# Performance work log

Measured on AMD Instinct MI355X. Metric: run time of the kernel, lower is better.

## Reference

```python
import jax, jax.numpy as jnp
import numpy as np

# LeNet-5 custom connectivity between S2 (6 ch) and C3 (16 ch): MAP[i, o] = 1 if input ch i feeds output ch o
MAP_INFO = np.array([
    [1, 0, 0, 0, 1, 1, 1, 0, 0, 1, 1, 1, 1, 0, 1, 1],
    [1, 1, 0, 0, 0, 1, 1, 1, 0, 0, 1, 1, 1, 1, 0, 1],
    [1, 1, 1, 0, 0, 0, 1, 1, 1, 0, 0, 1, 0, 1, 1, 1],
    [0, 1, 1, 1, 0, 0, 1, 1, 1, 1, 0, 0, 1, 0, 1, 1],
    [0, 0, 1, 1, 1, 0, 0, 1, 1, 1, 1, 0, 1, 1, 0, 1],
    [0, 0, 0, 1, 1, 1, 0, 0, 1, 1, 1, 1, 0, 1, 1, 1],
], dtype=np.float32)  # [6, 16]

SCALE = 1.7159
SLOPE = 2.0 / 3.0


def _conv(x, w):
    # x: [B, Cin, H, W], w: [Cout, Cin, kh, kw], VALID padding, stride 1
    return jax.lax.conv_general_dilated(
        x, w, window_strides=(1, 1), padding='VALID',
        dimension_numbers=('NCHW', 'OIHW', 'NCHW'))


def _subsample(x, w, b):
    # 2x2 average pool then per-channel affine (trainable scale/bias)
    B, C, H, W = x.shape
    p = x.reshape(B, C, H // 2, 2, W // 2, 2).mean(axis=(3, 5))
    return p * w[None, :, None, None] + b[None, :, None, None]


def _act(x):
    return SCALE * jnp.tanh(SLOPE * x)


def setup_inputs() -> dict:
    key = jax.random.key(0)
    ks = jax.random.split(key, 16)
    B = 8192

    def unif(k, shape, fan_in):
        return (jax.random.uniform(k, shape, dtype=jnp.float32) * 4.8 - 2.4) / fan_in

    x = jax.random.normal(ks[0], (B, 1, 32, 32), dtype=jnp.float32)
    c1_w = unif(ks[1], (6, 1, 5, 5), 25 * 1)
    c1_b = jax.random.uniform(ks[2], (6,), dtype=jnp.float32) * 0.1
    s2_w = unif(ks[3], (6,), 4)
    s2_b = jax.random.uniform(ks[4], (6,), dtype=jnp.float32)
    c3_w = unif(ks[5], (16, 6, 5, 5), 25 * 6)
    c3_b = jax.random.uniform(ks[6], (16,), dtype=jnp.float32) * 0.1
    s4_w = unif(ks[7], (16,), 4)
    s4_b = jax.random.uniform(ks[8], (16,), dtype=jnp.float32)
    c5_w = unif(ks[9], (120, 16, 5, 5), 25 * 16)
    c5_b = jax.random.uniform(ks[10], (120,), dtype=jnp.float32) * 0.1
    f6_w = unif(ks[11], (84, 120), 120)
    f6_b = jax.random.uniform(ks[12], (84,), dtype=jnp.float32) * 0.1
    rbf_w = jax.random.uniform(ks[13], (84, 10), dtype=jnp.float32)
    return dict(x=x, c1_w=c1_w, c1_b=c1_b, s2_w=s2_w, s2_b=s2_b,
                c3_w=c3_w, c3_b=c3_b, s4_w=s4_w, s4_b=s4_b,
                c5_w=c5_w, c5_b=c5_b, f6_w=f6_w, f6_b=f6_b, rbf_w=rbf_w)


def reference(x, c1_w, c1_b, s2_w, s2_b, c3_w, c3_b, s4_w, s4_b,
              c5_w, c5_b, f6_w, f6_b, rbf_w):
    # C1: 1->6 conv5, replicate padding 2 -> [B,6,32,32]
    xp = jnp.pad(x, ((0, 0), (0, 0), (2, 2), (2, 2)), mode='edge')
    h = _conv(xp, c1_w) + c1_b[None, :, None, None]
    # S2 + squashing act -> [B,6,16,16]
    h = _act(_subsample(h, s2_w, s2_b))
    # C3: sparse-connectivity conv expressed as dense conv with masked weights -> [B,16,12,12]
    mask = jnp.asarray(MAP_INFO.T)[:, :, None, None]  # [16,6,1,1]
    h = _conv(h, c3_w * mask) + c3_b[None, :, None, None]
    # S4 + act -> [B,16,6,6]
    h = _act(_subsample(h, s4_w, s4_b))
    # C5: 16->120 conv5 -> [B,120,1,1]
    h = _conv(h, c5_w) + c5_b[None, :, None, None]
    h = h.reshape(-1, 120)
    # F6 + act -> [B,84]
    h = _act(h @ f6_w.T + f6_b)
    # RBF output: squared euclidean distance to class prototypes -> [B,10]
    out = jnp.sum((h[:, :, None] - rbf_w[None, :, :]) ** 2, axis=1)
    return out
```

## Files before the change

### kernel.cpp

```cpp
#include <hip/hip_runtime.h>
#include <math.h>

typedef _Float16 h16;
typedef h16  h8v __attribute__((ext_vector_type(8)));
typedef h16  h4v __attribute__((ext_vector_type(4)));
typedef h16  h2v __attribute__((ext_vector_type(2)));
typedef float f4v __attribute__((ext_vector_type(4)));
typedef unsigned int u32;

#define WS_B1   0
#define WS_B3   8
#define WS_KB1  24
#define WS_W3H  408
#define WS_W5H  2712
#define WS_F6H  29336
#define WS_RBFH 35480
#define WS_PSQ  36248

#define L_B3    0
#define L_C5B   64
#define L_F6B   544
#define L_S2H   880
#define L_A5    880
#define L_HBH   880
#define L_XPAD  14704
#define L_S4    14704
#define L_A6    14704
#define L_GUARD 19888
#define LDS_TOTAL 20080

__device__ const unsigned char MASK16[16] = {7,14,28,56,49,35,15,30,60,57,51,39,27,54,45,63};

__device__ __forceinline__ float squash(float x) {
    float E = __expf(1.33333333f * x);
    return 1.7159f - 3.4318f * __builtin_amdgcn_rcpf(1.0f + E);
}

__device__ __forceinline__ void slot_to_uv(int c, int& u, int& v) {
    u = -1; v = 0;
    if (c < 32) {
        int q = c >> 3, j = c & 7;
        if (j < 6)       { u = q;     v = j; }
        else if (q == 2) { u = 4;     v = j - 6; }
        else if (q == 3) { u = 5;     v = j - 6; }
    } else {
        int cc = c - 32, q = cc >> 2, j = cc & 3;
        if (q == 0)      { u = 4;     v = 2 + j; }
        else if (q == 1) { u = 5;     v = 2 + j; }
    }
}

__global__ __launch_bounds__(256) void prep_kernel(
    const float* __restrict__ c1_w, const float* __restrict__ c1_b,
    const float* __restrict__ s2_w, const float* __restrict__ s2_b,
    const float* __restrict__ c3_w, const float* __restrict__ c3_b,
    const float* __restrict__ s4_w, const float* __restrict__ s4_b,
    const float* __restrict__ c5_w, const float* __restrict__ f6_w,
    const float* __restrict__ rbf_w,
    float* __restrict__ ws)
{
    const int gid = blockIdx.x * 256 + threadIdx.x;
    const int gstr = gridDim.x * 256;
    if (gid < 6)  ws[WS_B1 + gid] = s2_w[gid] * c1_b[gid] + s2_b[gid];
    if (gid < 16) ws[WS_B3 + gid] = s4_w[gid] * c3_b[gid] + s4_b[gid];
    h16* KB1 = (h16*)(ws + WS_KB1);
    for (int idx = gid; idx < 768; idx += gstr) {
        int n = idx / 48, c = idx - n * 48;
        int u, v; slot_to_uv(c, u, v);
        float val = 0.f;
        if (n < 6 && u >= 0) {
            float s = 0.f;
            #pragma unroll
            for (int dy = 0; dy < 2; ++dy)
                #pragma unroll
                for (int dx = 0; dx < 2; ++dx) {
                    int ky = u - dy, kx = v - dx;
                    if (ky >= 0 && ky < 5 && kx >= 0 && kx < 5)
                        s += c1_w[(n * 5 + ky) * 5 + kx];
                }
            val = 0.25f * s * s2_w[n];
        }
        KB1[idx] = (h16)val;
    }
    h16* W3H = (h16*)(ws + WS_W3H);
    for (int idx = gid; idx < 4608; idx += gstr) {
        int i = idx / 768, r = idx - i * 768;
        int n = r / 48, c = r - n * 48;
        int u, v; slot_to_uv(c, u, v);
        float val = 0.f;
        if (u >= 0) {
            float s = 0.f;
            #pragma unroll
            for (int dy = 0; dy < 2; ++dy)
                #pragma unroll
                for (int dx = 0; dx < 2; ++dx) {
                    int ky = u - dy, kx = v - dx;
                    if (ky >= 0 && ky < 5 && kx >= 0 && kx < 5)
                        s += c3_w[((n * 6 + i) * 5 + ky) * 5 + kx];
                }
            val = ((MASK16[n] >> i) & 1) ? 0.25f * s4_w[n] * s : 0.f;
        }
        W3H[idx] = (h16)val;
    }
    h16* W5H = (h16*)(ws + WS_W5H);
    for (int idx = gid; idx < 53248; idx += gstr) {
        int kb = idx >> 12, rr = idx & 4095;
        int n = rr >> 5, k = rr & 31;
        int kg = kb * 32 + k;
        int i = kg / 26, r = kg - i * 26;
        float val = (n < 120 && r < 25) ? c5_w[n * 400 + i * 25 + r] : 0.f;
        W5H[idx] = (h16)val;
    }
    h16* F6H = (h16*)(ws + WS_F6H);
    for (int idx = gid; idx < 12288; idx += gstr) {
        int n = idx >> 7, k = idx & 127;
        float val = (n < 84 && k < 120) ? f6_w[n * 120 + k] : 0.f;
        F6H[idx] = (h16)val;
    }
    h16* RBFH = (h16*)(ws + WS_RBFH);
    for (int idx = gid; idx < 1536; idx += gstr) {
        int n = idx / 96, k = idx - n * 96;
        float val = (n < 10 && k < 84) ? -2.f * rbf_w[k * 10 + n] : 0.f;
        RBFH[idx] = (h16)val;
    }
    if (gid < 10) {
        float s = 0.f;
        for (int k = 0; k < 84; ++k) {
            float pv = (float)(h16)rbf_w[k * 10 + gid];
            s += pv * pv;
        }
        ws[WS_PSQ + gid] = s;
    }
}

__global__ __launch_bounds__(256, 8) void lenet_kernel(
    const float* __restrict__ x,
    const float* __restrict__ c5_b, const float* __restrict__ f6_b,
    const float* __restrict__ ws,
    float* __restrict__ out)
{
    __shared__ __align__(16) char smem[LDS_TOTAL];
    float* s_b3  = (float*)(smem + L_B3);
    float* s_c5b = (float*)(smem + L_C5B);
    float* s_f6b = (float*)(smem + L_F6B);
    h16*  XPAD   = (h16*)(smem + L_XPAD);
    h16*  S2H    = (h16*)(smem + L_S2H);
    h16*  S4     = (h16*)(smem + L_S4);
    h16*  A5     = (h16*)(smem + L_A5);
    h16*  A6     = (h16*)(smem + L_A6);
    h16*  HBH    = (h16*)(smem + L_HBH);

    const int tid  = threadIdx.x;
    const int wave = __builtin_amdgcn_readfirstlane(tid >> 6);
    const int lane = tid & 63;
    const int quad = lane >> 4;
    const int lr   = lane & 15;

    if (tid < 16)  s_b3[tid] = ws[WS_B3 + tid];
    if (tid < 120) s_c5b[tid] = c5_b[tid];
    if (tid < 84)  s_f6b[tid] = f6_b[tid];
    if (tid < 48)  ((u32*)(smem + L_GUARD))[tid] = 0u;
    const float* xb = x + (size_t)blockIdx.x * 4096;
    const h16* KB1 = (const h16*)(ws + WS_KB1);
    h8v w1a = *(const h8v*)(KB1 + lr * 48 + quad * 8);
    h4v w1b = *(const h4v*)(KB1 + lr * 48 + 32 + quad * 4);
    float b1v = ws[WS_B1 + (lr < 6 ? lr : 0)];
    float psqv = ws[WS_PSQ + (lr < 10 ? lr : 0)];

    auto stageA = [&](int s) {
        #pragma unroll
        for (int k = 0; k < 2; ++k) {
            int idx = tid + k * 256;
            int im = idx >> 8;
            int r  = (idx >> 3) & 31;
            int c4 = idx & 7;
            float4 v = *(const float4*)(xb + (2 * s + im) * 1024 + r * 32 + c4 * 4);
            h2v p0; p0.x = (h16)v.x; p0.y = (h16)v.y;
            h2v p1; p1.x = (h16)v.z; p1.y = (h16)v.w;
            h16* d = XPAD + im * 1296 + (r + 2) * 36 + (4 * c4 + 2);
            *(h2v*)(d)     = p0;
            *(h2v*)(d + 2) = p1;
        }
        #pragma unroll
        for (int k = 0; k < 3; ++k) {
            int e = tid + k * 256;
            if (e < 544) {
                int im = (e >= 272) ? 1 : 0;
                int h = e - 272 * im;
                int u, v;
                if (h < 144) { int q = h / 36; u = (q < 2) ? q : 32 + q; v = h - q * 36; }
                else { int g = h - 144; u = 2 + (g >> 2); int q = g & 3; v = (q < 2) ? q : 32 + q; }
                int sr = min(max(u - 2, 0), 31), sc = min(max(v - 2, 0), 31);
                XPAD[im * 1296 + u * 36 + v] = (h16)xb[(2 * s + im) * 1024 + sr * 32 + sc];
            }
        }
    };

    auto stageB = [&](int s) {
        const h16* bp = XPAD + (wave >> 1) * 1296 + (wave & 1) * 576 + 2 * lr;
        h16* s2base = S2H + (s * 2 + (wave >> 1)) * 1728 + lr * 288 + (wave & 1) * 144 + quad * 4;
        #pragma unroll
        for (int tt = 0; tt < 8; ++tt) {
            const u32* bq = (const u32*)bp + quad * 18;
            union { u32 u[4]; h8v h; } av;
            av.u[0] = bq[0];  av.u[1] = bq[1];
            av.u[2] = bq[2];  av.u[3] = bq[36];
            f4v acc = {b1v, b1v, b1v, b1v};
            acc = __builtin_amdgcn_mfma_f32_16x16x32_f16(av.h, w1a, acc, 0, 0, 0);
            union { u32 u[2]; h4v h; } av2;
            av2.u[0] = bq[73]; av2.u[1] = bq[74];
            acc = __builtin_amdgcn_mfma_f32_16x16x16f16(av2.h, w1b, acc, 0, 0, 0);
            if (lr < 6) {
                h2v q0; q0.x = (h16)squash(acc[0]); q0.y = (h16)squash(acc[1]);
                h2v q1; q1.x = (h16)squash(acc[2]); q1.y = (h16)squash(acc[3]);
                *(h2v*)(s2base + tt * 18)     = q0;
                *(h2v*)(s2base + tt * 18 + 2) = q1;
            }
            bp += 72;
        }
    };

    stageA(0);
    __syncthreads();
    stageB(0);
    __syncthreads();
    stageA(1);
    __syncthreads();
    stageB(1);
    __syncthreads();

    f4v cacc0, cacc1, cacc2;
    const bool w0 = (wave == 0);
    {
        const h16* W3H = (const h16*)(ws + WS_W3H);
        int baseh0, baseh1, baseh2;
        {
            int m0 = wave * 16 + lr;
            int i0 = m0 / 36, p0 = m0 - i0 * 36;
            baseh0 = i0 * 1728 + (2 * (p0 / 6)) * 18 + 2 * (p0 % 6);
            int m1 = (wave + 4) * 16 + lr;
            int i1 = m1 / 36, p1 = m1 - i1 * 36;
            baseh1 = i1 * 1728 + (2 * (p1 / 6)) * 18 + 2 * (p1 % 6);
            int m2 = 128 + lr;
            int i2 = m2 / 36, p2 = m2 - i2 * 36;
            baseh2 = i2 * 1728 + (2 * (p2 / 6)) * 18 + 2 * (p2 % 6);
        }
        float b3v = s_b3[lr];
        f4v cinit = {b3v, b3v, b3v, b3v};
        cacc0 = cinit; cacc1 = cinit; cacc2 = cinit;
        #pragma unroll
        for (int i = 0; i < 6; ++i) {
            const h16* bbase = W3H + i * 768 + lr * 48;
            h8v w3a = *(const h8v*)(bbase + quad * 8);
            h4v w3b = *(const h4v*)(bbase + 32 + quad * 4);
            {
                const u32* cq = (const u32*)(S2H + baseh0 + i * 288) + quad * 9;
                union { u32 u[4]; h8v h; } av;
                av.u[0] = cq[0];  av.u[1] = cq[1];
                av.u[2] = cq[2];  av.u[3] = cq[18];
                cacc0 = __builtin_amdgcn_mfma_f32_16x16x32_f16(av.h, w3a, cacc0, 0, 0, 0);
                union { u32 u[2]; h4v h; } av2;
                av2.u[0] = cq[37]; av2.u[1] = cq[38];
                cacc0 = __builtin_amdgcn_mfma_f32_16x16x16f16(av2.h, w3b, cacc0, 0, 0, 0);
            }
            {
                const u32* cq = (const u32*)(S2H + baseh1 + i * 288) + quad * 9;
                union { u32 u[4]; h8v h; } av;
                av.u[0] = cq[0];  av.u[1] = cq[1];
                av.u[2] = cq[2];  av.u[3] = cq[18];
                cacc1 = __builtin_amdgcn_mfma_f32_16x16x32_f16(av.h, w3a, cacc1, 0, 0, 0);
                union { u32 u[2]; h4v h; } av2;
                av2.u[0] = cq[37]; av2.u[1] = cq[38];
                cacc1 = __builtin_amdgcn_mfma_f32_16x16x16f16(av2.h, w3b, cacc1, 0, 0, 0);
            }
            if (w0) {
                const u32* cq = (const u32*)(S2H + baseh2 + i * 288) + quad * 9;
                union { u32 u[4]; h8v h; } av;
                av.u[0] = cq[0];  av.u[1] = cq[1];
                av.u[2] = cq[2];  av.u[3] = cq[18];
                cacc2 = __builtin_amdgcn_mfma_f32_16x16x32_f16(av.h, w3a, cacc2, 0, 0, 0);
                union { u32 u[2]; h4v h; } av2;
                av2.u[0] = cq[37]; av2.u[1] = cq[38];
                cacc2 = __builtin_amdgcn_mfma_f32_16x16x16f16(av2.h, w3b, cacc2, 0, 0, 0);
            }
        }
    }

    const h16* W5H = (const h16*)(ws + WS_W5H);
    h8v bf0c = *(const h8v*)(W5H + (wave * 32 + lr) * 32 + quad * 8);
    h8v bf1c = *(const h8v*)(W5H + (wave * 32 + 16 + lr) * 32 + quad * 8);

    {
        #pragma unroll
        for (int r = 0; r < 4; ++r) {
            int m = wave * 16 + quad * 4 + r;
            int img = m / 36, pos = m - img * 36;
            S4[img * 672 + lr * 42 + pos] = (h16)squash(cacc0[r]);
        }
        #pragma unroll
        for (int r = 0; r < 4; ++r) {
            int m = (wave + 4) * 16 + quad * 4 + r;
            int img = m / 36, pos = m - img * 36;
            S4[img * 672 + lr * 42 + pos] = (h16)squash(cacc1[r]);
        }
        if (w0) {
            #pragma unroll
            for (int r = 0; r < 4; ++r) {
                int m = 128 + quad * 4 + r;
                int img = m / 36, pos = m - img * 36;
                S4[img * 672 + lr * 42 + pos] = (h16)squash(cacc2[r]);
            }
        }
    }
    __syncthreads();

    {
        int m = tid >> 4, i = tid & 15;
        int img = m >> 2, q = m & 3, qy = q >> 1, qx = q & 1;
        const h16* s4b = S4 + img * 672 + i * 42 + qy * 6 + qx;
        u32* dst = (u32*)(A5 + m * 424 + i * 26);
        #pragma unroll
        for (int w = 0; w < 12; ++w) {
            int k0 = 2 * w, k1 = 2 * w + 1;
            union { h2v h; u32 u; } p;
            p.h.x = s4b[(k0 / 5) * 6 + (k0 % 5)];
            p.h.y = s4b[(k1 / 5) * 6 + (k1 % 5)];
            dst[w] = p.u;
        }
        {
            union { h2v h; u32 u; } p;
            p.h.x = s4b[28];
            p.h.y = (h16)0.f;
            dst[12] = p.u;
        }
    }
    __syncthreads();

    {
        h8v af0c = *(const h8v*)(A5 + lr * 424 + quad * 8);
        float c5b0 = s_c5b[wave * 32 + lr];
        float c5b1 = s_c5b[wave * 32 + 16 + lr];
        f4v dacc0 = {c5b0, c5b0, c5b0, c5b0};
        f4v dacc1 = {c5b1, c5b1, c5b1, c5b1};
        #pragma unroll
        for (int i = 0; i < 13; ++i) {
            h8v bf0n, bf1n, af0n;
            if (i < 12) {
                bf0n = *(const h8v*)(W5H + (i + 1) * 4096 + (wave * 32 + lr) * 32 + quad * 8);
                bf1n = *(const h8v*)(W5H + (i + 1) * 4096 + (wave * 32 + 16 + lr) * 32 + quad * 8);
                af0n = *(const h8v*)(A5 + lr * 424 + (i + 1) * 32 + quad * 8);
            }
            dacc0 = __builtin_amdgcn_mfma_f32_16x16x32_f16(af0c, bf0c, dacc0, 0, 0, 0);
            dacc1 = __builtin_amdgcn_mfma_f32_16x16x32_f16(af0c, bf1c, dacc1, 0, 0, 0);
            if (i < 12) { bf0c = bf0n; bf1c = bf1n; af0c = af0n; }
        }
        if (tid < 64) {
            int m = tid >> 2, j = tid & 3;
            *(u32*)(A6 + m * 136 + 120 + 2 * j) = 0u;
        }
        {
            int n0 = wave * 32 + lr;
            if (n0 < 120) {
                int tt = n0 / 30, cb = (n0 - tt * 30) * 4;
                #pragma unroll
                for (int r = 0; r < 4; ++r) {
                    int m = quad * 4 + r;
                    A6[((m >> 2) * 4 + tt) * 136 + cb + (m & 3)] = (h16)dacc0[r];
                }
            }
            int n1 = wave * 32 + 16 + lr;
            if (n1 < 120) {
                int tt = n1 / 30, cb = (n1 - tt * 30) * 4;
                #pragma unroll
                for (int r = 0; r < 4; ++r) {
                    int m = quad * 4 + r;
                    A6[((m >> 2) * 4 + tt) * 136 + cb + (m & 3)] = (h16)dacc1[r];
                }
            }
        }
    }

    const h16* F6H = (const h16*)(ws + WS_F6H);
    const int wv2 = (wave < 2) ? wave + 4 : wave;
    h8v eb0c = *(const h8v*)(F6H + (wave * 16 + lr) * 128 + quad * 8);
    h8v eb1c = *(const h8v*)(F6H + (wv2 * 16 + lr) * 128 + quad * 8);
    __syncthreads();

    if (tid < 96) {
        int m = tid / 6, j = tid - m * 6;
        ((u32*)HBH)[m * 48 + 42 + j] = 0u;
    }

    {
        h8v a8c = *(const h8v*)(A6 + lr * 136 + quad * 8);
        float f60 = s_f6b[wave * 16 + lr];
        f4v eacc0 = {f60, f60, f60, f60};
        f4v eacc1 = {};
        const bool w2 = (wave < 2);
        if (w2) {
            int n1 = (wave + 4) * 16 + lr;
            float f61 = (n1 < 84) ? s_f6b[n1] : 0.f;
            eacc1[0] = f61; eacc1[1] = f61; eacc1[2] = f61; eacc1[3] = f61;
        }
        #pragma unroll
        for (int kc = 0; kc < 4; ++kc) {
            h8v eb0n, eb1n, a8n;
            if (kc < 3) {
                eb0n = *(const h8v*)(F6H + (wave * 16 + lr) * 128 + (kc + 1) * 32 + quad * 8);
                eb1n = *(const h8v*)(F6H + (wv2 * 16 + lr) * 128 + (kc + 1) * 32 + quad * 8);
                a8n  = *(const h8v*)(A6 + lr * 136 + (kc + 1) * 32 + quad * 8);
            }
            eacc0 = __builtin_amdgcn_mfma_f32_16x16x32_f16(a8c, eb0c, eacc0, 0, 0, 0);
            if (w2)
                eacc1 = __builtin_amdgcn_mfma_f32_16x16x32_f16(a8c, eb1c, eacc1, 0, 0, 0);
            if (kc < 3) { eb0c = eb0n; eb1c = eb1n; a8c = a8n; }
        }
        {
            int n = wave * 16 + lr;
            #pragma unroll
            for (int r = 0; r < 4; ++r) {
                int m = quad * 4 + r;
                HBH[m * 96 + n] = (h16)squash(eacc0[r]);
            }
        }
        if (w2) {
            int n = (wave + 4) * 16 + lr;
            if (n < 84) {
                #pragma unroll
                for (int r = 0; r < 4; ++r) {
                    int m = quad * 4 + r;
                    HBH[m * 96 + n] = (h16)squash(eacc1[r]);
                }
            }
        }
    }
    __syncthreads();

    if (w0) {
        const h16* RBFH = (const h16*)(ws + WS_RBFH);
        h8v gb0 = *(const h8v*)(RBFH + lr * 96 + quad * 8);
        h8v gb1 = *(const h8v*)(RBFH + lr * 96 + 32 + quad * 8);
        h8v gb2 = *(const h8v*)(RBFH + lr * 96 + 64 + quad * 8);
        h8v ga0 = *(const h8v*)(HBH + lr * 96 + quad * 8);
        h8v ga1 = *(const h8v*)(HBH + lr * 96 + 32 + quad * 8);
        h8v ga2 = *(const h8v*)(HBH + lr * 96 + 64 + quad * 8);
        f4v hh = {};
        hh = __builtin_amdgcn_mfma_f32_16x16x32_f16(ga0, ga0, hh, 0, 0, 0);
        hh = __builtin_amdgcn_mfma_f32_16x16x32_f16(ga1, ga1, hh, 0, 0, 0);
        hh = __builtin_amdgcn_mfma_f32_16x16x32_f16(ga2, ga2, hh, 0, 0, 0);
        f4v d2 = {psqv, psqv, psqv, psqv};
        d2 = __builtin_amdgcn_mfma_f32_16x16x32_f16(ga0, gb0, d2, 0, 0, 0);
        d2 = __builtin_amdgcn_mfma_f32_16x16x32_f16(ga1, gb1, d2, 0, 0, 0);
        d2 = __builtin_amdgcn_mfma_f32_16x16x32_f16(ga2, gb2, d2, 0, 0, 0);
        float* ob = out + (size_t)blockIdx.x * 160;
        #pragma unroll
        for (int r = 0; r < 4; ++r) {
            float hsq = __shfl(hh[r], quad * 20 + r);
            if (lr < 10)
                ob[(quad * 4 + r) * 10 + lr] = hsq + d2[r];
        }
    }
}

extern "C" void kernel_launch(void* const* d_in, const int* in_sizes, int n_in,
                              void* d_out, int out_size, void* d_ws, size_t ws_size,
                              hipStream_t stream) {
    (void)n_in; (void)out_size; (void)ws_size;
    const float* x     = (const float*)d_in[0];
    const float* c1_w  = (const float*)d_in[1];
    const float* c1_b  = (const float*)d_in[2];
    const float* s2_w  = (const float*)d_in[3];
    const float* s2_b  = (const float*)d_in[4];
    const float* c3_w  = (const float*)d_in[5];
    const float* c3_b  = (const float*)d_in[6];
    const float* s4_w  = (const float*)d_in[7];
    const float* s4_b  = (const float*)d_in[8];
    const float* c5_w  = (const float*)d_in[9];
    const float* c5_b  = (const float*)d_in[10];
    const float* f6_w  = (const float*)d_in[11];
    const float* f6_b  = (const float*)d_in[12];
    const float* rbf_w = (const float*)d_in[13];
    float* out = (float*)d_out;
    float* ws  = (float*)d_ws;

    const int B = in_sizes[0] / 1024;

    prep_kernel<<<256, 256, 0, stream>>>(c1_w, c1_b, s2_w, s2_b, c3_w, c3_b,
                                         s4_w, s4_b, c5_w, f6_w, rbf_w, ws);
    lenet_kernel<<<B / 4, 256, 0, stream>>>(x, c5_b, f6_b, ws, out);
}
```

Before: 132.6 us.

## Feed C5 MFMA directly from transposed S4 layout, dropping im2col staging pass

Stores the S4 activations channel-minor (pos*16+channel) and reorganises the C5 weights per kernel tap, so the C5 GEMM reads its A fragments straight from S4 with 16x16x16 MFMAs over 25 taps. This removes the separate im2col copy into A5 and one block barrier. It also moves the RBF weight loads ahead of the final barrier so they overlap it. The cost is twice as many, smaller MFMAs and 8-byte loads in place of 16-byte ones, plus a new LDS layout with different bank-conflict behaviour.

```diff
diff --git a/kernel.cpp b/kernel.cpp
--- a/kernel.cpp
+++ b/kernel.cpp
@@ -12,20 +12,19 @@
 #define WS_B3   8
 #define WS_KB1  24
 #define WS_W3H  408
-#define WS_W5H  2712
-#define WS_F6H  29336
-#define WS_RBFH 35480
-#define WS_PSQ  36248
+#define WS_W5T  2712
+#define WS_F6H  28312
+#define WS_RBFH 34456
+#define WS_PSQ  35224
 
 #define L_B3    0
 #define L_C5B   64
 #define L_F6B   544
 #define L_S2H   880
-#define L_A5    880
-#define L_HBH   880
+#define L_A6    880
+#define L_HBH   5232
 #define L_XPAD  14704
-#define L_S4    14704
-#define L_A6    14704
+#define L_S4T   14704
 #define L_GUARD 19888
 #define LDS_TOTAL 20080
 
@@ -102,14 +101,13 @@
         }
         W3H[idx] = (h16)val;
     }
-    h16* W5H = (h16*)(ws + WS_W5H);
-    for (int idx = gid; idx < 53248; idx += gstr) {
-        int kb = idx >> 12, rr = idx & 4095;
-        int n = rr >> 5, k = rr & 31;
-        int kg = kb * 32 + k;
-        int i = kg / 26, r = kg - i * 26;
-        float val = (n < 120 && r < 25) ? c5_w[n * 400 + i * 25 + r] : 0.f;
-        W5H[idx] = (h16)val;
+    h16* W5T = (h16*)(ws + WS_W5T);
+    for (int idx = gid; idx < 51200; idx += gstr) {
+        int rc = idx >> 11;
+        int rr = idx & 2047;
+        int n = rr >> 4, i = rr & 15;
+        float val = (n < 120) ? c5_w[n * 400 + i * 25 + rc] : 0.f;
+        W5T[idx] = (h16)val;
     }
     h16* F6H = (h16*)(ws + WS_F6H);
     for (int idx = gid; idx < 12288; idx += gstr) {
@@ -145,8 +143,7 @@
     float* s_f6b = (float*)(smem + L_F6B);
     h16*  XPAD   = (h16*)(smem + L_XPAD);
     h16*  S2H    = (h16*)(smem + L_S2H);
-    h16*  S4     = (h16*)(smem + L_S4);
-    h16*  A5     = (h16*)(smem + L_A5);
+    h16*  S4T    = (h16*)(smem + L_S4T);
     h16*  A6     = (h16*)(smem + L_A6);
     h16*  HBH    = (h16*)(smem + L_HBH);
 
@@ -286,77 +283,61 @@
         }
     }
 
-    const h16* W5H = (const h16*)(ws + WS_W5H);
-    h8v bf0c = *(const h8v*)(W5H + (wave * 32 + lr) * 32 + quad * 8);
-    h8v bf1c = *(const h8v*)(W5H + (wave * 32 + 16 + lr) * 32 + quad * 8);
+    const h16* W5T = (const h16*)(ws + WS_W5T);
+    const h16* wb0 = W5T + (wave * 32 + lr) * 16 + quad * 4;
+    const h16* wb1 = W5T + (wave * 32 + 16 + lr) * 16 + quad * 4;
+    h4v b0c = *(const h4v*)(wb0);
+    h4v b1c = *(const h4v*)(wb1);
 
     {
         #pragma unroll
         for (int r = 0; r < 4; ++r) {
             int m = wave * 16 + quad * 4 + r;
             int img = m / 36, pos = m - img * 36;
-            S4[img * 672 + lr * 42 + pos] = (h16)squash(cacc0[r]);
+            S4T[img * 584 + pos * 16 + lr] = (h16)squash(cacc0[r]);
         }
         #pragma unroll
         for (int r = 0; r < 4; ++r) {
             int m = (wave + 4) * 16 + quad * 4 + r;
             int img = m / 36, pos = m - img * 36;
-            S4[img * 672 + lr * 42 + pos] = (h16)squash(cacc1[r]);
+            S4T[img * 584 + pos * 16 + lr] = (h16)squash(cacc1[r]);
         }
         if (w0) {
             #pragma unroll
             for (int r = 0; r < 4; ++r) {
                 int m = 128 + quad * 4 + r;
                 int img = m / 36, pos = m - img * 36;
-                S4[img * 672 + lr * 42 + pos] = (h16)squash(cacc2[r]);
+                S4T[img * 584 + pos * 16 + lr] = (h16)squash(cacc2[r]);
             }
         }
     }
     __syncthreads();
 
     {
-        int m = tid >> 4, i = tid & 15;
-        int img = m >> 2, q = m & 3, qy = q >> 1, qx = q & 1;
-        const h16* s4b = S4 + img * 672 + i * 42 + qy * 6 + qx;
-        u32* dst = (u32*)(A5 + m * 424 + i * 26);
-        #pragma unroll
-        for (int w = 0; w < 12; ++w) {
-            int k0 = 2 * w, k1 = 2 * w + 1;
-            union { h2v h; u32 u; } p;
-            p.h.x = s4b[(k0 / 5) * 6 + (k0 % 5)];
-            p.h.y = s4b[(k1 / 5) * 6 + (k1 % 5)];
-            dst[w] = p.u;
-        }
-        {
-            union { h2v h; u32 u; } p;
-            p.h.x = s4b[28];
-            p.h.y = (h16)0.f;
-            dst[12] = p.u;
-        }
-    }
-    __syncthreads();
-
-    {
-        h8v af0c = *(const h8v*)(A5 + lr * 424 + quad * 8);
+        int img_ = lr >> 2, q_ = lr & 3;
+        const h16* s4b = S4T + img_ * 584 + ((q_ >> 1) * 6 + (q_ & 1)) * 16 + quad * 4;
+        if (tid < 64) {
+            int m = tid >> 2, j = tid & 3;
+            *(u32*)(A6 + m * 136 + 120 + 2 * j) = 0u;
+        }
         float c5b0 = s_c5b[wave * 32 + lr];
         float c5b1 = s_c5b[wave * 32 + 16 + lr];
         f4v dacc0 = {c5b0, c5b0, c5b0, c5b0};
         f4v dacc1 = {c5b1, c5b1, c5b1, c5b1};
-        #pragma unroll
-        for (int i = 0; i < 13; ++i) {
-            h8v bf0n, bf1n, af0n;
-            if (i < 12) {
-                bf0n = *(const h8v*)(W5H + (i + 1) * 4096 + (wave * 32 + lr) * 32 + quad * 8);
-                bf1n = *(const h8v*)(W5H + (i + 1) * 4096 + (wave * 32 + 16 + lr) * 32 + quad * 8);
-                af0n = *(const h8v*)(A5 + lr * 424 + (i + 1) * 32 + quad * 8);
-            }
-            dacc0 = __builtin_amdgcn_mfma_f32_16x16x32_f16(af0c, bf0c, dacc0, 0, 0, 0);
-            dacc1 = __builtin_amdgcn_mfma_f32_16x16x32_f16(af0c, bf1c, dacc1, 0, 0, 0);
-            if (i < 12) { bf0c = bf0n; bf1c = bf1n; af0c = af0n; }
-        }
-        if (tid < 64) {
-            int m = tid >> 2, j = tid & 3;
-            *(u32*)(A6 + m * 136 + 120 + 2 * j) = 0u;
+        h4v a_c = *(const h4v*)(s4b);
+        #pragma unroll
+        for (int rc = 0; rc < 25; ++rc) {
+            h4v a_n, b0n, b1n;
+            if (rc < 24) {
+                int nr = rc + 1;
+                int off = ((nr / 5) * 6 + (nr % 5)) * 16;
+                a_n = *(const h4v*)(s4b + off);
+                b0n = *(const h4v*)(wb0 + (rc + 1) * 2048);
+                b1n = *(const h4v*)(wb1 + (rc + 1) * 2048);
+            }
+            dacc0 = __builtin_amdgcn_mfma_f32_16x16x16f16(a_c, b0c, dacc0, 0, 0, 0);
+            dacc1 = __builtin_amdgcn_mfma_f32_16x16x16f16(a_c, b1c, dacc1, 0, 0, 0);
+            if (rc < 24) { a_c = a_n; b0c = b0n; b1c = b1n; }
         }
         {
             int n0 = wave * 32 + lr;
@@ -434,13 +415,17 @@
             }
         }
     }
-    __syncthreads();
-
+
+    h8v gb0, gb1, gb2;
     if (w0) {
         const h16* RBFH = (const h16*)(ws + WS_RBFH);
-        h8v gb0 = *(const h8v*)(RBFH + lr * 96 + quad * 8);
-        h8v gb1 = *(const h8v*)(RBFH + lr * 96 + 32 + quad * 8);
-        h8v gb2 = *(const h8v*)(RBFH + lr * 96 + 64 + quad * 8);
+        gb0 = *(const h8v*)(RBFH + lr * 96 + quad * 8);
+        gb1 = *(const h8v*)(RBFH + lr * 96 + 32 + quad * 8);
+        gb2 = *(const h8v*)(RBFH + lr * 96 + 64 + quad * 8);
+    }
+    __syncthreads();
+
+    if (w0) {
         h8v ga0 = *(const h8v*)(HBH + lr * 96 + quad * 8);
         h8v ga1 = *(const h8v*)(HBH + lr * 96 + 32 + quad * 8);
         h8v ga2 = *(const h8v*)(HBH + lr * 96 + 64 + quad * 8);
```

Result: no change. 130.9 us (-1.3%).
